# Performance work log

Hardware: AMD Instinct MI355X
Metric: run time of the kernel (lower is better)

## Reference

```python
import jax, jax.numpy as jnp
import numpy as np
from jax import lax

B, S = 32, 256
V, D = 32000, 300   # pretrained word embeddings
P, PD = 35, 32      # pos vocab / pos embed dim (from source)
M = 66              # morph feature dim
H = 6               # LSTM units per direction -> bilstm_output_size = 12
A = 12


def _lstm(x, Wx, Wh, b, reverse=False):
    # x: [B,S,F] -> h: [B,S,H]; keras gate order i,f,c,o
    xg = x @ Wx + b  # precompute input projection once: [B,S,4H]
    def step(carry, xt):
        h, c = carry
        g = xt + h @ Wh
        i, f, cand, o = jnp.split(g, 4, axis=-1)
        c = jax.nn.sigmoid(f) * c + jax.nn.sigmoid(i) * jnp.tanh(cand)
        h = jax.nn.sigmoid(o) * jnp.tanh(c)
        return (h, c), h
    h0 = jnp.zeros((x.shape[0], Wh.shape[0]), x.dtype)
    _, hs = lax.scan(step, (h0, h0), jnp.swapaxes(xg, 0, 1), reverse=reverse)
    return jnp.swapaxes(hs, 0, 1)


def setup_inputs() -> dict:
    key = jax.random.key(0)
    ks = jax.random.split(key, 16)
    F = D + PD + M
    n = lambda k, shp, s=0.1: jax.random.normal(k, shp, dtype=jnp.float32) * s
    return {
        'words': jax.random.randint(ks[0], (B, S), 0, V),
        'pos': jax.random.randint(ks[1], (B, S), 0, P),
        'morph': jax.random.uniform(ks[2], (B, S, M), dtype=jnp.float32),
        'heads': jax.random.randint(ks[3], (B, S), 0, S),
        'word_table': n(ks[4], (V, D)),
        'pos_table': n(ks[5], (P, PD)),
        'Wx_f': n(ks[6], (F, 4 * H)), 'Wh_f': n(ks[7], (H, 4 * H)), 'b_f': jnp.zeros((4 * H,), jnp.float32),
        'Wx_b': n(ks[8], (F, 4 * H)), 'Wh_b': n(ks[9], (H, 4 * H)), 'b_b': jnp.zeros((4 * H,), jnp.float32),
        'Wu': n(ks[10], (A, A)), 'bu': jnp.zeros((A,), jnp.float32),
        'Ww': n(ks[11], (A, A)), 'bw': jnp.zeros((A,), jnp.float32),
        'v': n(ks[12], (A,)),
    }


def reference(words, pos, morph, heads, word_table, pos_table,
              Wx_f, Wh_f, b_f, Wx_b, Wh_b, b_b, Wu, bu, Ww, bw, v):
    # embed + concat -> [B,S,F]
    feats = jnp.concatenate([word_table[words], pos_table[pos], morph], axis=-1)
    # BiLSTM encoder -> [B,S,12] (dropout disabled / eval)
    hf = _lstm(feats, Wx_f, Wh_f, b_f)
    hb = _lstm(feats, Wx_b, Wh_b, b_b, reverse=True)
    repr_ = jnp.concatenate([hf, hb], axis=-1)
    # Bahdanau arc scoring, vectorized over dependant i (the tf loop):
    # scores[b,i,j] = v . tanh(u_a(repr)[b,j] + w_a(repr)[b,i])
    ua = repr_ @ Wu + bu  # head-position term (j)
    wa = repr_ @ Ww + bw  # dependant term (i)
    scores = jnp.einsum('bijd,d->bij', jnp.tanh(ua[:, None, :, :] + wa[:, :, None, :]), v)
    # the equality-based mask in tf picks out j == i (self cannot be head)
    eye = jnp.eye(S, dtype=bool)
    scores = jnp.where(eye[None], -10000.0, scores)
    # per-step sparse CE (from_logits, mean over batch), summed over i=1..S-1
    logp = jax.nn.log_softmax(scores, axis=-1)
    ce = -jnp.take_along_axis(logp, heads[:, :, None], axis=2)[..., 0]  # [B,S]
    loss = jnp.sum(jnp.mean(ce[:, 1:], axis=0))
    # parent_prob_table: exp(scores) concatenated along axis 0, i-major as in tf loop
    table = jnp.swapaxes(jnp.exp(scores[:, 1:, :]), 0, 1).reshape((S - 1) * B, S)
    return loss, table
```

## Files before the change

kernel.cpp:

```cpp
#include <hip/hip_runtime.h>
#include <hip/hip_bf16.h>

#define BB 32
#define SS 256
#define DD 300
#define PDD 32
#define MM 66
#define FF 398
#define HH 6
#define G4 24
#define AA 12

__device__ __forceinline__ float fast_rcp(float x) { return __builtin_amdgcn_rcpf(x); }
__device__ __forceinline__ float fast_tanh(float x) {
    return 1.f - 2.f * fast_rcp(__expf(2.f * x) + 1.f);
}
__device__ __forceinline__ float bcast_lane(float x, int l) {
    return __int_as_float(__builtin_amdgcn_readlane(__float_as_int(x), l));
}
__device__ __forceinline__ float bperm(int byteaddr, float v) {
    return __int_as_float(__builtin_amdgcn_ds_bpermute(byteaddr, __float_as_int(v)));
}

#define EP_POS 32
__global__ __launch_bounds__(256) void k_embed_proj(
    const int* __restrict__ words, const int* __restrict__ pos,
    const float* __restrict__ morph, const float* __restrict__ wtab,
    const float* __restrict__ ptab,
    const float* __restrict__ Wxf, const float* __restrict__ bfv,
    const float* __restrict__ Wxb, const float* __restrict__ bbv,
    float* __restrict__ xgf, float* __restrict__ xgb)
{
    __shared__ float sfeat[EP_POS * 100];
    __shared__ float sW[48 * 100];

    int t   = threadIdx.x;
    int bs0 = blockIdx.x * EP_POS;

    int cg   = t & 15;
    int slot = t >> 4;
    float a00 = 0.f, a01 = 0.f, a02 = 0.f;
    float a10 = 0.f, a11 = 0.f, a12 = 0.f;

    for (int tile = 0; tile < 4; ++tile) {
        if (tile < 3) {
            for (int idx = t; idx < EP_POS * 25; idx += 256) {
                int pp = idx / 25, f = idx % 25;
                const float4* srcr = (const float4*)(wtab +
                    (size_t)words[bs0 + pp] * DD + tile * 100);
                ((float4*)sfeat)[pp * 25 + f] = srcr[f];
            }
        } else {
            for (int idx = t; idx < EP_POS * 100; idx += 256) {
                int pp = idx / 100, kk = idx % 100;
                float vv;
                if (kk < PDD)           vv = ptab[pos[bs0 + pp] * PDD + kk];
                else if (kk < PDD + MM) vv = morph[(size_t)(bs0 + pp) * MM + (kk - PDD)];
                else                    vv = 0.f;
                sfeat[pp * 100 + kk] = vv;
            }
        }
        for (int idx = t; idx < 2400; idx += 256) {
            int kk = idx / 24, j = idx % 24;
            int k = tile * 100 + kk;
            float wf = (k < FF) ? Wxf[k * G4 + j] : 0.f;
            float wb = (k < FF) ? Wxb[k * G4 + j] : 0.f;
            sW[j * 100 + kk]        = wf;
            sW[(24 + j) * 100 + kk] = wb;
        }
        __syncthreads();

        const float4* F0 = (const float4*)(sfeat + slot * 100);
        const float4* F1 = (const float4*)(sfeat + (slot + 16) * 100);
        const float4* W0 = (const float4*)(sW + (3 * cg + 0) * 100);
        const float4* W1 = (const float4*)(sW + (3 * cg + 1) * 100);
        const float4* W2 = (const float4*)(sW + (3 * cg + 2) * 100);
        #pragma unroll 5
        for (int q = 0; q < 25; ++q) {
            float4 f0 = F0[q], f1 = F1[q];
            float4 w0 = W0[q], w1 = W1[q], w2 = W2[q];
            a00 = fmaf(f0.x, w0.x, a00); a00 = fmaf(f0.y, w0.y, a00);
            a00 = fmaf(f0.z, w0.z, a00); a00 = fmaf(f0.w, w0.w, a00);
            a01 = fmaf(f0.x, w1.x, a01); a01 = fmaf(f0.y, w1.y, a01);
            a01 = fmaf(f0.z, w1.z, a01); a01 = fmaf(f0.w, w1.w, a01);
            a02 = fmaf(f0.x, w2.x, a02); a02 = fmaf(f0.y, w2.y, a02);
            a02 = fmaf(f0.z, w2.z, a02); a02 = fmaf(f0.w, w2.w, a02);
            a10 = fmaf(f1.x, w0.x, a10); a10 = fmaf(f1.y, w0.y, a10);
            a10 = fmaf(f1.z, w0.z, a10); a10 = fmaf(f1.w, w0.w, a10);
            a11 = fmaf(f1.x, w1.x, a11); a11 = fmaf(f1.y, w1.y, a11);
            a11 = fmaf(f1.z, w1.z, a11); a11 = fmaf(f1.w, w1.w, a11);
            a12 = fmaf(f1.x, w2.x, a12); a12 = fmaf(f1.y, w2.y, a12);
            a12 = fmaf(f1.z, w2.z, a12); a12 = fmaf(f1.w, w2.w, a12);
        }
        __syncthreads();
    }

    int c0  = 3 * cg;
    int dir = c0 >= 24 ? 1 : 0;
    int jj  = c0 - dir * 24;
    const float* bias = dir ? bbv : bfv;
    float*       xg   = dir ? xgb : xgf;
    float b0 = bias[jj], b1 = bias[jj + 1], b2 = bias[jj + 2];
    float* o0 = xg + (size_t)(bs0 + slot) * G4 + jj;
    float* o1 = xg + (size_t)(bs0 + slot + 16) * G4 + jj;
    o0[0] = a00 + b0; o0[1] = a01 + b1; o0[2] = a02 + b2;
    o1[0] = a10 + b0; o1[1] = a11 + b1; o1[2] = a12 + b2;
}

__global__ __launch_bounds__(64) void k_lstm(
    const float* __restrict__ xgf, const float* __restrict__ xgb,
    const float* __restrict__ Whf, const float* __restrict__ Whb,
    float* __restrict__ repr)
{
    __shared__ float sxg[(SS + 8) * G4];
    __shared__ float hbuf[SS * HH];
    int blk = blockIdx.x;
    int dir = blk >> 5;
    int b   = blk & 31;
    int lane = threadIdx.x;

    const float* xg = (dir ? xgb : xgf) + (size_t)b * SS * G4;
    const float* Wh = dir ? Whb : Whf;

    {
        const float4* src = (const float4*)xg;
        float4* dst = (float4*)sxg;
        #pragma unroll
        for (int u = 0; u < 24; ++u) {
            int d = lane + u * 64;
            int row = d / 6, col = d - row * 6;
            int drow = dir ? (SS - 1 - row) : row;
            dst[drow * 6 + col] = src[d];
        }
        for (int g = lane; g < 8 * G4; g += 64) sxg[SS * G4 + g] = 0.f;
    }

    int j    = lane % G4;
    int cell = lane % HH;
    int type = j / HH;

    float wh[HH];
    #pragma unroll
    for (int m = 0; m < HH; ++m) wh[m] = Wh[m * G4 + j];

    const float L2E = 1.4426950408889634f;
    float kk = (type == 2) ? 2.f * L2E : -L2E;
    float Bc = (type == 2) ? 1.f : 0.f;
    float Ac = (type == 2) ? -1.f : 1.f;

    int ai = cell * 4;
    int af = (HH + cell) * 4;
    int ac = (2 * HH + cell) * 4;
    int ao = (3 * HH + cell) * 4;

    float sh[HH];
    #pragma unroll
    for (int m = 0; m < HH; ++m) sh[m] = 0.f;
    float c = 0.f;
    __syncthreads();

    const float* xb = sxg + j;

    float pg[4];
    #pragma unroll
    for (int sl = 0; sl < 4; ++sl) pg[sl] = xb[sl * G4];

    #pragma unroll 1
    for (int t = 0; t < SS; t += 4) {
        #pragma unroll
        for (int sl = 0; sl < 4; ++sl) {
            float x = pg[sl];
            pg[sl] = xb[(t + 4 + sl) * G4];

            #pragma unroll
            for (int m = 0; m < HH; ++m) x = fmaf(sh[m], wh[m], x);

            float e  = __builtin_amdgcn_exp2f(x * kk);
            float vv = fmaf(Bc, e, Ac) * fast_rcp(1.f + e);

            float vi = bperm(ai, vv);
            float vf = bperm(af, vv);
            float vc = bperm(ac, vv);
            float vo = bperm(ao, vv);

            c = fmaf(vf, c, vi * vc);
            float ec = __builtin_amdgcn_exp2f(c * (2.f * L2E));
            float h  = (ec - 1.f) * fast_rcp(ec + 1.f) * vo;

            hbuf[(t + sl) * HH + cell] = h;
            #pragma unroll
            for (int m = 0; m < HH; ++m) sh[m] = bcast_lane(h, m);
        }
    }
    __syncthreads();

    #pragma unroll
    for (int u = 0; u < (SS * HH) / 64; ++u) {
        int idx = lane + u * 64;
        int tt = idx / 6, cc = idx - tt * 6;
        int s = dir ? (SS - 1 - tt) : tt;
        repr[((size_t)b * SS + s) * (2 * HH) + dir * HH + cc] = hbuf[idx];
    }
}

__global__ __launch_bounds__(256) void k_uawa(
    const float* __restrict__ repr,
    const float* __restrict__ Wu, const float* __restrict__ bu,
    const float* __restrict__ Ww, const float* __restrict__ bw,
    float* __restrict__ ua, float* __restrict__ wa)
{
    int bs = blockIdx.x * blockDim.x + threadIdx.x;
    float r[AA];
    #pragma unroll
    for (int e = 0; e < AA; ++e) r[e] = repr[(size_t)bs * AA + e];
    #pragma unroll
    for (int d = 0; d < AA; ++d) {
        float au = bu[d], aw = bw[d];
        #pragma unroll
        for (int e = 0; e < AA; ++e) {
            au = fmaf(r[e], Wu[e * AA + d], au);
            aw = fmaf(r[e], Ww[e * AA + d], aw);
        }
        ua[(size_t)bs * AA + d] = au;
        wa[(size_t)bs * AA + d] = aw;
    }
}

__global__ __launch_bounds__(256) void k_score(
    const float* __restrict__ ua, const float* __restrict__ wa,
    const float* __restrict__ v, const int* __restrict__ heads,
    float* __restrict__ out, float* __restrict__ ce)
{
    int bi = blockIdx.x;
    int i  = bi & 255;
    int j  = threadIdx.x;

    __shared__ float swa[AA], sv[AA];
    if (j < AA) { swa[j] = wa[(size_t)bi * AA + j]; sv[j] = v[j]; }
    __syncthreads();

    const float* uj = ua + ((size_t)(bi & ~255) + j) * AA;
    float s = 0.f;
    #pragma unroll
    for (int d = 0; d < AA; ++d) s = fmaf(sv[d], fast_tanh(uj[d] + swa[d]), s);
    if (j == i) s = -10000.f;

    float e = __expf(s);
    if (i >= 1)
        out[1 + (((size_t)(i - 1) * BB + (bi >> 8)) * SS + j)] = e;

    float r = e;
    #pragma unroll
    for (int off = 32; off > 0; off >>= 1) r += __shfl_xor(r, off, 64);
    __shared__ float part[4];
    if ((j & 63) == 0) part[j >> 6] = r;
    __syncthreads();
    float tot = part[0] + part[1] + part[2] + part[3];

    if (j == heads[bi])
        ce[bi] = (i >= 1) ? (__logf(tot) - s) : 0.f;
}

__global__ __launch_bounds__(256) void k_loss(const float* __restrict__ ce,
                                              float* __restrict__ out)
{
    __shared__ float red[256];
    int t = threadIdx.x;
    float a = 0.f;
    for (int k = t; k < BB * SS; k += 256) a += ce[k];
    red[t] = a; __syncthreads();
    for (int off = 128; off > 0; off >>= 1) {
        if (t < off) red[t] += red[t + off];
        __syncthreads();
    }
    if (t == 0) out[0] = red[0] * (1.f / BB);
}

extern "C" void kernel_launch(void* const* d_in, const int* in_sizes, int n_in,
                              void* d_out, int out_size, void* d_ws, size_t ws_size,
                              hipStream_t stream)
{
    const int*   words = (const int*)  d_in[0];
    const int*   pos   = (const int*)  d_in[1];
    const float* morph = (const float*)d_in[2];
    const int*   heads = (const int*)  d_in[3];
    const float* wtab  = (const float*)d_in[4];
    const float* ptab  = (const float*)d_in[5];
    const float* Wxf   = (const float*)d_in[6];
    const float* Whf   = (const float*)d_in[7];
    const float* bf    = (const float*)d_in[8];
    const float* Wxb   = (const float*)d_in[9];
    const float* Whb   = (const float*)d_in[10];
    const float* bb    = (const float*)d_in[11];
    const float* Wu    = (const float*)d_in[12];
    const float* bu    = (const float*)d_in[13];
    const float* Ww    = (const float*)d_in[14];
    const float* bw    = (const float*)d_in[15];
    const float* v     = (const float*)d_in[16];
    float* out = (float*)d_out;

    float* xgf  = (float*)d_ws;
    float* xgb  = xgf  + (size_t)BB*SS*G4;
    float* repr = xgb  + (size_t)BB*SS*G4;
    float* ua   = repr + (size_t)BB*SS*2*HH;
    float* wa   = ua   + (size_t)BB*SS*AA;
    float* ce   = wa   + (size_t)BB*SS*AA;

    k_embed_proj<<<(BB * SS) / EP_POS, 256, 0, stream>>>(words, pos, morph, wtab, ptab,
                                                         Wxf, bf, Wxb, bb, xgf, xgb);
    k_lstm<<<BB * 2, 64, 0, stream>>>(xgf, xgb, Whf, Whb, repr);
    k_uawa<<<(BB * SS) / 256, 256, 0, stream>>>(repr, Wu, bu, Ww, bw, ua, wa);
    k_score<<<BB * SS, 256, 0, stream>>>(ua, wa, v, heads, out, ce);
    k_loss<<<1, 256, 0, stream>>>(ce, out);
}
```

Measured before the change: 86.41 us.

## Split embedding projection into gather and GEMV kernels; use DPP gate exchange in LSTM

The fused embed+projection kernel is replaced by two kernels. The first gathers the concatenated features into a padded 400-wide global buffer and writes transposed input weights. The second computes the per-gate projections, one wave per six gate columns. In the LSTM recurrence, gates are laid out so each cell's i/f/c/o sit in one lane quad. DPP quad broadcasts replace LDS bpermutes on the serial critical path, and the exp2 scale factors are folded into the inputs and recurrent weights ahead of time. The cost is an extra global write and read of the roughly 13 MB feature buffer plus one more kernel launch.

```diff
diff --git a/kernel.cpp b/kernel.cpp
--- a/kernel.cpp
+++ b/kernel.cpp
@@ -10,6 +10,7 @@
 #define HH 6
 #define G4 24
 #define AA 12
+#define L2E 1.4426950408889634f
 
 __device__ __forceinline__ float fast_rcp(float x) { return __builtin_amdgcn_rcpf(x); }
 __device__ __forceinline__ float fast_tanh(float x) {
@@ -18,93 +19,79 @@
 __device__ __forceinline__ float bcast_lane(float x, int l) {
     return __int_as_float(__builtin_amdgcn_readlane(__float_as_int(x), l));
 }
-__device__ __forceinline__ float bperm(int byteaddr, float v) {
-    return __int_as_float(__builtin_amdgcn_ds_bpermute(byteaddr, __float_as_int(v)));
-}
-
-#define EP_POS 32
-__global__ __launch_bounds__(256) void k_embed_proj(
+template<int CTRL>
+__device__ __forceinline__ float quad_bcast(float v) {
+    return __int_as_float(__builtin_amdgcn_mov_dpp(__float_as_int(v), CTRL, 0xf, 0xf, true));
+}
+
+__global__ __launch_bounds__(256) void k_prep(
     const int* __restrict__ words, const int* __restrict__ pos,
     const float* __restrict__ morph, const float* __restrict__ wtab,
     const float* __restrict__ ptab,
-    const float* __restrict__ Wxf, const float* __restrict__ bfv,
-    const float* __restrict__ Wxb, const float* __restrict__ bbv,
+    const float* __restrict__ Wxf, const float* __restrict__ Wxb,
+    float* __restrict__ feats, float* __restrict__ WT)
+{
+    int t  = threadIdx.x;
+    int pl = t >> 4;
+    int ln = t & 15;
+    int p  = blockIdx.x * 16 + pl;
+
+    float* frow = feats + (size_t)p * 400;
+    float4* f4  = (float4*)frow;
+    const float4* ws4 = (const float4*)(wtab + (size_t)words[p] * DD);
+    for (int k4 = ln; k4 < 75; k4 += 16) f4[k4] = ws4[k4];
+    const float4* ps4 = (const float4*)(ptab + pos[p] * PDD);
+    if (ln < 8) f4[75 + ln] = ps4[ln];
+    const float2* ms2 = (const float2*)(morph + (size_t)p * MM);
+    float2* f2 = (float2*)frow;
+    for (int k2 = ln; k2 < 33; k2 += 16) f2[166 + k2] = ms2[k2];
+    if (ln == 0) f2[199] = make_float2(0.f, 0.f);
+
+    if (blockIdx.x < 2) {
+        const float* Wx = blockIdx.x ? Wxb : Wxf;
+        float* wt = WT + blockIdx.x * (G4 * 400);
+        for (int idx = t; idx < G4 * 400; idx += 256) {
+            int jj = idx / 400, k = idx % 400;
+            wt[idx] = (k < FF) ? Wx[k * G4 + jj] : 0.f;
+        }
+    }
+}
+
+__global__ __launch_bounds__(256) void k_xg(
+    const float* __restrict__ feats, const float* __restrict__ WT,
+    const float* __restrict__ bfv, const float* __restrict__ bbv,
     float* __restrict__ xgf, float* __restrict__ xgb)
 {
-    __shared__ float sfeat[EP_POS * 100];
-    __shared__ float sW[48 * 100];
-
-    int t   = threadIdx.x;
-    int bs0 = blockIdx.x * EP_POS;
-
-    int cg   = t & 15;
-    int slot = t >> 4;
-    float a00 = 0.f, a01 = 0.f, a02 = 0.f;
-    float a10 = 0.f, a11 = 0.f, a12 = 0.f;
-
-    for (int tile = 0; tile < 4; ++tile) {
-        if (tile < 3) {
-            for (int idx = t; idx < EP_POS * 25; idx += 256) {
-                int pp = idx / 25, f = idx % 25;
-                const float4* srcr = (const float4*)(wtab +
-                    (size_t)words[bs0 + pp] * DD + tile * 100);
-                ((float4*)sfeat)[pp * 25 + f] = srcr[f];
-            }
-        } else {
-            for (int idx = t; idx < EP_POS * 100; idx += 256) {
-                int pp = idx / 100, kk = idx % 100;
-                float vv;
-                if (kk < PDD)           vv = ptab[pos[bs0 + pp] * PDD + kk];
-                else if (kk < PDD + MM) vv = morph[(size_t)(bs0 + pp) * MM + (kk - PDD)];
-                else                    vv = 0.f;
-                sfeat[pp * 100 + kk] = vv;
-            }
-        }
-        for (int idx = t; idx < 2400; idx += 256) {
-            int kk = idx / 24, j = idx % 24;
-            int k = tile * 100 + kk;
-            float wf = (k < FF) ? Wxf[k * G4 + j] : 0.f;
-            float wb = (k < FF) ? Wxb[k * G4 + j] : 0.f;
-            sW[j * 100 + kk]        = wf;
-            sW[(24 + j) * 100 + kk] = wb;
-        }
-        __syncthreads();
-
-        const float4* F0 = (const float4*)(sfeat + slot * 100);
-        const float4* F1 = (const float4*)(sfeat + (slot + 16) * 100);
-        const float4* W0 = (const float4*)(sW + (3 * cg + 0) * 100);
-        const float4* W1 = (const float4*)(sW + (3 * cg + 1) * 100);
-        const float4* W2 = (const float4*)(sW + (3 * cg + 2) * 100);
-        #pragma unroll 5
-        for (int q = 0; q < 25; ++q) {
-            float4 f0 = F0[q], f1 = F1[q];
-            float4 w0 = W0[q], w1 = W1[q], w2 = W2[q];
-            a00 = fmaf(f0.x, w0.x, a00); a00 = fmaf(f0.y, w0.y, a00);
-            a00 = fmaf(f0.z, w0.z, a00); a00 = fmaf(f0.w, w0.w, a00);
-            a01 = fmaf(f0.x, w1.x, a01); a01 = fmaf(f0.y, w1.y, a01);
-            a01 = fmaf(f0.z, w1.z, a01); a01 = fmaf(f0.w, w1.w, a01);
-            a02 = fmaf(f0.x, w2.x, a02); a02 = fmaf(f0.y, w2.y, a02);
-            a02 = fmaf(f0.z, w2.z, a02); a02 = fmaf(f0.w, w2.w, a02);
-            a10 = fmaf(f1.x, w0.x, a10); a10 = fmaf(f1.y, w0.y, a10);
-            a10 = fmaf(f1.z, w0.z, a10); a10 = fmaf(f1.w, w0.w, a10);
-            a11 = fmaf(f1.x, w1.x, a11); a11 = fmaf(f1.y, w1.y, a11);
-            a11 = fmaf(f1.z, w1.z, a11); a11 = fmaf(f1.w, w1.w, a11);
-            a12 = fmaf(f1.x, w2.x, a12); a12 = fmaf(f1.y, w2.y, a12);
-            a12 = fmaf(f1.z, w2.z, a12); a12 = fmaf(f1.w, w2.w, a12);
-        }
-        __syncthreads();
-    }
-
-    int c0  = 3 * cg;
-    int dir = c0 >= 24 ? 1 : 0;
-    int jj  = c0 - dir * 24;
+    int tile = blockIdx.x >> 1;
+    int half = blockIdx.x & 1;
+    int wave = threadIdx.x >> 6;
+    int lane = threadIdx.x & 63;
+    int cg   = __builtin_amdgcn_readfirstlane(half * 4 + wave);
+    int dir  = cg >> 2;
+    int j0   = (cg & 3) * 6;
+    int pp   = tile * 64 + lane;
+
+    const float4* fp4 = (const float4*)(feats + (size_t)pp * 400);
+    const float*  wt0 = WT + dir * (G4 * 400) + j0 * 400;
+
+    float acc[6] = {0.f, 0.f, 0.f, 0.f, 0.f, 0.f};
+    #pragma unroll 8
+    for (int q = 0; q < 100; ++q) {
+        float4 f = fp4[q];
+        #pragma unroll
+        for (int c2 = 0; c2 < 6; ++c2) {
+            const float4 w = *(const float4*)(wt0 + c2 * 400 + q * 4);
+            acc[c2] = fmaf(f.x, w.x, acc[c2]);
+            acc[c2] = fmaf(f.y, w.y, acc[c2]);
+            acc[c2] = fmaf(f.z, w.z, acc[c2]);
+            acc[c2] = fmaf(f.w, w.w, acc[c2]);
+        }
+    }
     const float* bias = dir ? bbv : bfv;
-    float*       xg   = dir ? xgb : xgf;
-    float b0 = bias[jj], b1 = bias[jj + 1], b2 = bias[jj + 2];
-    float* o0 = xg + (size_t)(bs0 + slot) * G4 + jj;
-    float* o1 = xg + (size_t)(bs0 + slot + 16) * G4 + jj;
-    o0[0] = a00 + b0; o0[1] = a01 + b1; o0[2] = a02 + b2;
-    o1[0] = a10 + b0; o1[1] = a11 + b1; o1[2] = a12 + b2;
+    float2* o2 = (float2*)((dir ? xgb : xgf) + (size_t)pp * G4 + j0);
+    o2[0] = make_float2(acc[0] + bias[j0 + 0], acc[1] + bias[j0 + 1]);
+    o2[1] = make_float2(acc[2] + bias[j0 + 2], acc[3] + bias[j0 + 3]);
+    o2[2] = make_float2(acc[4] + bias[j0 + 4], acc[5] + bias[j0 + 5]);
 }
 
 __global__ __launch_bounds__(64) void k_lstm(
@@ -128,35 +115,36 @@
         #pragma unroll
         for (int u = 0; u < 24; ++u) {
             int d = lane + u * 64;
-            int row = d / 6, col = d - row * 6;
+            int row = d / 6, c4 = d - row * 6;
             int drow = dir ? (SS - 1 - row) : row;
-            dst[drow * 6 + col] = src[d];
-        }
-        for (int g = lane; g < 8 * G4; g += 64) sxg[SS * G4 + g] = 0.f;
-    }
-
-    int j    = lane % G4;
-    int cell = lane % HH;
-    int type = j / HH;
-
+            float4 v = src[d];
+            int cb = c4 * 4;
+            v.x *= (cb + 0 >= 12 && cb + 0 < 18) ? 2.f * L2E : -L2E;
+            v.y *= (cb + 1 >= 12 && cb + 1 < 18) ? 2.f * L2E : -L2E;
+            v.z *= (cb + 2 >= 12 && cb + 2 < 18) ? 2.f * L2E : -L2E;
+            v.w *= (cb + 3 >= 12 && cb + 3 < 18) ? 2.f * L2E : -L2E;
+            dst[drow * 6 + c4] = v;
+        }
+        for (int g2 = lane; g2 < 8 * G4; g2 += 64) sxg[SS * G4 + g2] = 0.f;
+    }
+
+    int g    = lane % G4;
+    int cell = g >> 2;
+    int type = g & 3;
+    int j    = type * HH + cell;
+
+    float kk = (type == 2) ? 2.f * L2E : -L2E;
     float wh[HH];
     #pragma unroll
-    for (int m = 0; m < HH; ++m) wh[m] = Wh[m * G4 + j];
-
-    const float L2E = 1.4426950408889634f;
-    float kk = (type == 2) ? 2.f * L2E : -L2E;
+    for (int m = 0; m < HH; ++m) wh[m] = Wh[m * G4 + j] * kk;
     float Bc = (type == 2) ? 1.f : 0.f;
     float Ac = (type == 2) ? -1.f : 1.f;
 
-    int ai = cell * 4;
-    int af = (HH + cell) * 4;
-    int ac = (2 * HH + cell) * 4;
-    int ao = (3 * HH + cell) * 4;
-
     float sh[HH];
     #pragma unroll
     for (int m = 0; m < HH; ++m) sh[m] = 0.f;
     float c = 0.f;
+    bool wr = (lane < G4) && ((lane & 3) == 0);
     __syncthreads();
 
     const float* xb = sxg + j;
@@ -172,24 +160,26 @@
             float x = pg[sl];
             pg[sl] = xb[(t + 4 + sl) * G4];
 
-            #pragma unroll
-            for (int m = 0; m < HH; ++m) x = fmaf(sh[m], wh[m], x);
-
-            float e  = __builtin_amdgcn_exp2f(x * kk);
-            float vv = fmaf(Bc, e, Ac) * fast_rcp(1.f + e);
-
-            float vi = bperm(ai, vv);
-            float vf = bperm(af, vv);
-            float vc = bperm(ac, vv);
-            float vo = bperm(ao, vv);
+            float aa  = fmaf(sh[1], wh[1], fmaf(sh[0], wh[0], x));
+            float bb2 = fmaf(sh[3], wh[3], sh[2] * wh[2]);
+            float cc2 = fmaf(sh[5], wh[5], sh[4] * wh[4]);
+            x = (aa + bb2) + cc2;
+
+            float e   = __builtin_amdgcn_exp2f(x);
+            float val = fmaf(Bc, e, Ac) * fast_rcp(1.f + e);
+
+            float vi = quad_bcast<0>(val);
+            float vf = quad_bcast<85>(val);
+            float vc = quad_bcast<170>(val);
+            float vo = quad_bcast<255>(val);
 
             c = fmaf(vf, c, vi * vc);
             float ec = __builtin_amdgcn_exp2f(c * (2.f * L2E));
             float h  = (ec - 1.f) * fast_rcp(ec + 1.f) * vo;
 
-            hbuf[(t + sl) * HH + cell] = h;
+            if (wr) hbuf[(t + sl) * HH + cell] = h;
             #pragma unroll
-            for (int m = 0; m < HH; ++m) sh[m] = bcast_lane(h, m);
+            for (int m = 0; m < HH; ++m) sh[m] = bcast_lane(h, 4 * m);
         }
     }
     __syncthreads();
@@ -299,15 +289,18 @@
     const float* v     = (const float*)d_in[16];
     float* out = (float*)d_out;
 
-    float* xgf  = (float*)d_ws;
-    float* xgb  = xgf  + (size_t)BB*SS*G4;
-    float* repr = xgb  + (size_t)BB*SS*G4;
-    float* ua   = repr + (size_t)BB*SS*2*HH;
-    float* wa   = ua   + (size_t)BB*SS*AA;
-    float* ce   = wa   + (size_t)BB*SS*AA;
-
-    k_embed_proj<<<(BB * SS) / EP_POS, 256, 0, stream>>>(words, pos, morph, wtab, ptab,
-                                                         Wxf, bf, Wxb, bb, xgf, xgb);
+    float* xgf   = (float*)d_ws;
+    float* xgb   = xgf   + (size_t)BB*SS*G4;
+    float* repr  = xgb   + (size_t)BB*SS*G4;
+    float* ua    = repr  + (size_t)BB*SS*2*HH;
+    float* wa    = ua    + (size_t)BB*SS*AA;
+    float* ce    = wa    + (size_t)BB*SS*AA;
+    float* feats = ce    + (size_t)BB*SS;
+    float* WT    = feats + (size_t)BB*SS*400;
+
+    k_prep<<<(BB * SS) / 16, 256, 0, stream>>>(words, pos, morph, wtab, ptab,
+                                               Wxf, Wxb, feats, WT);
+    k_xg<<<256, 256, 0, stream>>>(feats, WT, bf, bb, xgf, xgb);
     k_lstm<<<BB * 2, 64, 0, stream>>>(xgf, xgb, Whf, Whb, repr);
     k_uawa<<<(BB * SS) / 256, 256, 0, stream>>>(repr, Wu, bu, Ww, bw, ua, wa);
     k_score<<<BB * SS, 256, 0, stream>>>(ua, wa, v, heads, out, ce);
```

Measured after the change: 91.91 us. +6.4%, slower.
